# Kernel optimization log

Hardware: AMD Instinct MI355X
Metric: run time of the kernel (lower is better)

Reference implementation:

```python
import jax, jax.numpy as jnp
from jax import lax
import numpy as np

# Mask type 'A' for 7x7 conv: rows above center, left of center in center row; center excluded.
_m = np.zeros((7, 7), np.float32)
_m[:3, :] = 1.0
_m[3, :3] = 1.0
MASK_A = jnp.asarray(_m)


def masked_conv7(x, w, b):
    # x: [B,1,H,W], w: [16,1,7,7]
    wm = w * MASK_A[None, None]
    y = lax.conv_general_dilated(x, wm, (1, 1), [(3, 3), (3, 3)],
                                 dimension_numbers=("NCHW", "OIHW", "NCHW"))
    return y + b[None, :, None, None]


def skew(x):
    # [B,C,H,W] -> [B,C,H,H+W-1], row i shifted right by i (diagonals -> columns)
    B, C, H, W = x.shape
    rows = jnp.arange(H)[:, None]
    cols = rows + jnp.arange(W)[None, :]
    out = jnp.zeros((B, C, H, H + W - 1), x.dtype)
    return out.at[:, :, rows, cols].set(x)


def unskew(xs, W):
    B, C, H, _ = xs.shape
    rows = jnp.arange(H)[:, None]
    cols = rows + jnp.arange(W)[None, :]
    return xs[:, :, rows, cols]


def diag_lstm(x, wi, bi, ws0, ws1):
    # One direction of the diagonal LSTM. x: [B,16,H,W]
    B, C, H, W = x.shape
    xs = skew(x)  # [B,16,H,T], T = H+W-1
    # 1x1 input-to-state conv over the whole skewed map (precomputed)
    i2s = jnp.einsum("oc,bcht->boht", wi, xs) + bi[None, :, None, None]  # [B,64,H,T]

    def step(carry, col):
        h, c = carry  # [B,16,H] each
        # 2x1 state-to-state conv along height (causal downward): taps h[i], h[i-1]
        h_up = jnp.pad(h, ((0, 0), (0, 0), (1, 0)))[:, :, :-1]
        s = col + jnp.einsum("oc,bch->boh", ws1, h) + jnp.einsum("oc,bch->boh", ws0, h_up)
        o, f, i, g = jnp.split(s, 4, axis=1)
        c = jax.nn.sigmoid(f) * c + jax.nn.sigmoid(i) * jnp.tanh(g)
        h = jax.nn.sigmoid(o) * jnp.tanh(c)
        return (h, c), h

    cols = jnp.moveaxis(i2s, 3, 0)  # [T,B,64,H]
    z = jnp.zeros((B, C, H), x.dtype)
    _, hs = lax.scan(step, (z, z), cols)  # [T,B,16,H]
    hs = jnp.moveaxis(hs, 0, 3)  # [B,16,H,T]
    return unskew(hs, W)


def bilstm_layer(x, wi2, bi2, w02, w12):
    fwd = diag_lstm(x, wi2[0], bi2[0], w02[0], w12[0])
    xr = x[:, :, :, ::-1]
    bwd = diag_lstm(xr, wi2[1], bi2[1], w02[1], w12[1])[:, :, :, ::-1]
    # shift right-to-left output down one row to preserve causality
    bwd = jnp.pad(bwd, ((0, 0), (0, 0), (1, 0), (0, 0)))[:, :, :-1, :]
    return x + fwd + bwd  # residual


def pixelrnn_fwd(X, conv_in_w, conv_in_b, rnn_i2s_w, rnn_i2s_b, rnn_ss_w0, rnn_ss_w1,
                 out_w1, out_b1, out_w2, out_b2, out_w3, out_b3):
    h = masked_conv7(X, conv_in_w, conv_in_b)
    for l in range(7):
        h = bilstm_layer(h, rnn_i2s_w[l], rnn_i2s_b[l], rnn_ss_w0[l], rnn_ss_w1[l])
    for w, b in ((out_w1, out_b1), (out_w2, out_b2)):
        h = jax.nn.relu(jnp.einsum("oc,bchw->bohw", w, h) + b[None, :, None, None])
    return jnp.einsum("oc,bchw->bohw", out_w3, h) + out_b3[None, :, None, None]


def setup_inputs() -> dict:
    key = jax.random.key(0)
    ks = jax.random.split(key, 10)
    B, H, W = 32, 64, 64
    s = 0.25  # ~1/sqrt(16) init scale
    return {
        "X": jax.random.normal(ks[0], (B, 1, H, W), jnp.float32),
        "conv_in_w": jax.random.normal(ks[1], (16, 1, 7, 7), jnp.float32) * 0.15,
        "conv_in_b": jnp.zeros((16,), jnp.float32),
        "rnn_i2s_w": jax.random.normal(ks[2], (7, 2, 64, 16), jnp.float32) * s,
        "rnn_i2s_b": jnp.zeros((7, 2, 64), jnp.float32),
        "rnn_ss_w0": jax.random.normal(ks[3], (7, 2, 64, 16), jnp.float32) * s,
        "rnn_ss_w1": jax.random.normal(ks[4], (7, 2, 64, 16), jnp.float32) * s,
        "out_w1": jax.random.normal(ks[5], (16, 16), jnp.float32) * s,
        "out_b1": jnp.zeros((16,), jnp.float32),
        "out_w2": jax.random.normal(ks[6], (16, 16), jnp.float32) * s,
        "out_b2": jnp.zeros((16,), jnp.float32),
        "out_w3": jax.random.normal(ks[7], (1, 16), jnp.float32) * s,
        "out_b3": jnp.zeros((1,), jnp.float32),
    }


def reference(X, conv_in_w, conv_in_b, rnn_i2s_w, rnn_i2s_b, rnn_ss_w0, rnn_ss_w1,
              out_w1, out_b1, out_w2, out_b2, out_w3, out_b3):
    return pixelrnn_fwd(X, conv_in_w, conv_in_b, rnn_i2s_w, rnn_i2s_b, rnn_ss_w0,
                        rnn_ss_w1, out_w1, out_b1, out_w2, out_b2, out_w3, out_b3)
```

## Files before the change

kernel.cpp:

```cpp
#include <hip/hip_runtime.h>

#define DI __device__ __forceinline__

typedef __bf16 bf16x8 __attribute__((ext_vector_type(8)));
typedef float f32x4 __attribute__((ext_vector_type(4)));
typedef unsigned short u16x8 __attribute__((ext_vector_type(8)));
typedef unsigned short u16x4 __attribute__((ext_vector_type(4)));

DI float frcp(float x) { return __builtin_amdgcn_rcpf(x); }
DI float fsig(float x) { return frcp(1.0f + __expf(-x)); }
DI float ftanh(float x) { return 1.0f - 2.0f * frcp(1.0f + __expf(2.0f * x)); }

__global__ __launch_bounds__(256) void k_conv(const float* __restrict__ X,
                                              const float* __restrict__ Wc,
                                              const float* __restrict__ Bc,
                                              float* __restrict__ xo) {
    int n = blockIdx.x * 256 + threadIdx.x;
    int xx = n & 63, yy = (n >> 6) & 63, b = n >> 12;
    float acc[16];
#pragma unroll
    for (int o = 0; o < 16; ++o) acc[o] = Bc[o];
    const float* Xb = X + (size_t)b * 4096;
#pragma unroll
    for (int ky = 0; ky < 4; ++ky) {
        int yi = yy + ky - 3;
        if (yi < 0) continue;
        int kxmax = (ky == 3) ? 3 : 7;
        for (int kx = 0; kx < kxmax; ++kx) {
            int xi = xx + kx - 3;
            if (xi < 0 || xi > 63) continue;
            float v = Xb[yi * 64 + xi];
#pragma unroll
            for (int o = 0; o < 16; ++o)
                acc[o] = fmaf(Wc[o * 49 + ky * 7 + kx], v, acc[o]);
        }
    }
    float4* xp = reinterpret_cast<float4*>(xo + (size_t)n * 16);
#pragma unroll
    for (int q = 0; q < 4; ++q) {
        float4 t; t.x = acc[q*4]; t.y = acc[q*4+1]; t.z = acc[q*4+2]; t.w = acc[q*4+3];
        xp[q] = t;
    }
}

__global__ __launch_bounds__(256, 1) void k_scan(const float* __restrict__ Vin,
                                                 float* __restrict__ Vout,
                                                 const float* __restrict__ fwdIn,
                                                 const float* __restrict__ bwdIn,
                                                 float* __restrict__ fwdOut,
                                                 float* __restrict__ bwdOut,
                                                 const float* __restrict__ wi_all,
                                                 const float* __restrict__ w0_all,
                                                 const float* __restrict__ w1_all,
                                                 const float* __restrict__ bi_all,
                                                 int layer, int first) {
    int dir = blockIdx.x >> 5, b = blockIdx.x & 31;
    int t = threadIdx.x;
    int wv = t >> 6;
    int l = t & 63;
    int kb = l >> 4;
    int m = l & 15;
    int r = wv * 16 + m;
    int wb_ = (layer * 2 + dir) * 1024;

    const float* Wsel = (kb < 2 ? w1_all : w0_all) + wb_;
    int koff = (kb & 1) * 8;
    bf16x8 ahi[4], alo[4];
#pragma unroll
    for (int mb = 0; mb < 4; ++mb) {
        const float* wr = Wsel + (mb * 16 + m) * 16 + koff;
#pragma unroll
        for (int j = 0; j < 8; ++j) {
            float wv_ = wr[j];
            __bf16 hi = (__bf16)wv_;
            ahi[mb][j] = hi;
            alo[mb][j] = (__bf16)(wv_ - (float)hi);
        }
    }

    const float* Wi = wi_all + wb_;
    int cbase = (kb & 1) * 8;
    bf16x8 wihi[4], wiloz[4];
#pragma unroll
    for (int mb = 0; mb < 4; ++mb) {
        const float* wr = Wi + (mb * 16 + m) * 16 + cbase;
#pragma unroll
        for (int j = 0; j < 8; ++j) {
            float wv_ = wr[j];
            __bf16 hi = (__bf16)wv_;
            wihi[mb][j] = hi;
            wiloz[mb][j] = (kb < 2) ? (__bf16)(wv_ - (float)hi) : (__bf16)0.f;
        }
    }

    f32x4 biasv[4];
#pragma unroll
    for (int mb = 0; mb < 4; ++mb)
#pragma unroll
        for (int j = 0; j < 4; ++j)
            biasv[mb][j] = bi_all[(layer * 2 + dir) * 64 + mb * 16 + kb * 4 + j];

    __shared__ __align__(16) unsigned short hbuf[2][2][65 * 24];
    for (int i = t; i < 2 * 2 * 65 * 24; i += 256) (&hbuf[0][0][0])[i] = 0;

    const size_t rowbase  = ((size_t)b * 64 + r) * 64;
    const size_t rowbaseU = ((size_t)b * 64 + (r - 1)) * 64;
    float* ob = dir ? bwdOut : fwdOut;
    bool vstore_lane = (!first) && (dir == 0) && (kb < 2);
    bool fb_load = !first;
    bool b_load = fb_load && (r > 0);

    float cst[4] = {0.f, 0.f, 0.f, 0.f};

    f32x4 xc[2], fc[2], bc[2];
    {
        int w = 0 - r;
        bool valid = (unsigned)w < 64u;
#pragma unroll
        for (int q = 0; q < 2; ++q) { xc[q] = (f32x4){0,0,0,0}; fc[q] = (f32x4){0,0,0,0}; bc[q] = (f32x4){0,0,0,0}; }
        if (valid) {
            int wimg = dir ? (63 - w) : w;
            const f32x4* px = reinterpret_cast<const f32x4*>(Vin + (rowbase + wimg) * 16 + cbase);
            xc[0] = px[0]; xc[1] = px[1];
            if (fb_load) {
                const f32x4* pf = reinterpret_cast<const f32x4*>(fwdIn + (rowbase + wimg) * 16 + cbase);
                fc[0] = pf[0]; fc[1] = pf[1];
                if (b_load) {
                    const f32x4* pb = reinterpret_cast<const f32x4*>(bwdIn + (rowbaseU + wimg) * 16 + cbase);
                    bc[0] = pb[0]; bc[1] = pb[1];
                }
            }
        }
    }
    __syncthreads();

    int p = 0;
#pragma unroll 1
    for (int tt = 0; tt < 127; ++tt) {
        f32x4 xn[2], fn[2], bn[2];
#pragma unroll
        for (int q = 0; q < 2; ++q) { xn[q] = (f32x4){0,0,0,0}; fn[q] = (f32x4){0,0,0,0}; bn[q] = (f32x4){0,0,0,0}; }
        {
            int w = tt + 1 - r;
            if ((unsigned)w < 64u) {
                int wimg = dir ? (63 - w) : w;
                const f32x4* px = reinterpret_cast<const f32x4*>(Vin + (rowbase + wimg) * 16 + cbase);
                xn[0] = px[0]; xn[1] = px[1];
                if (fb_load) {
                    const f32x4* pf = reinterpret_cast<const f32x4*>(fwdIn + (rowbase + wimg) * 16 + cbase);
                    fn[0] = pf[0]; fn[1] = pf[1];
                    if (b_load) {
                        const f32x4* pb = reinterpret_cast<const f32x4*>(bwdIn + (rowbaseU + wimg) * 16 + cbase);
                        bn[0] = pb[0]; bn[1] = pb[1];
                    }
                }
            }
        }

        int wcur = tt - r;
        bool vout = (unsigned)wcur < 64u;
        int wo = dir ? (63 - wcur) : wcur;

        f32x4 v8[2];
#pragma unroll
        for (int q = 0; q < 2; ++q) v8[q] = xc[q] + fc[q] + bc[q];
        bf16x8 vsel;
#pragma unroll
        for (int q = 0; q < 2; ++q)
#pragma unroll
            for (int j = 0; j < 4; ++j) {
                float f = v8[q][j];
                __bf16 hi = (__bf16)f;
                vsel[q * 4 + j] = (kb < 2) ? hi : (__bf16)(f - (float)hi);
            }
        if (vstore_lane && vout) {
            f32x4* pv = reinterpret_cast<f32x4*>(Vout + (rowbase + wo) * 16 + cbase);
            pv[0] = v8[0]; pv[1] = v8[1];
        }

        f32x4 acc[4];
#pragma unroll
        for (int mb = 0; mb < 4; ++mb) acc[mb] = biasv[mb];
#pragma unroll
        for (int mb = 0; mb < 4; ++mb)
            acc[mb] = __builtin_amdgcn_mfma_f32_16x16x32_bf16(wihi[mb], vsel, acc[mb], 0, 0, 0);
#pragma unroll
        for (int mb = 0; mb < 4; ++mb)
            acc[mb] = __builtin_amdgcn_mfma_f32_16x16x32_bf16(wiloz[mb], vsel, acc[mb], 0, 0, 0);

        int q = r + 1 - (kb >> 1);
        int boff = q * 24 + (kb & 1) * 8;
        u16x8 bh_raw = *reinterpret_cast<const u16x8*>(&hbuf[p][0][boff]);
        u16x8 bl_raw = *reinterpret_cast<const u16x8*>(&hbuf[p][1][boff]);
        bf16x8 bhi = __builtin_bit_cast(bf16x8, bh_raw);
        bf16x8 blo = __builtin_bit_cast(bf16x8, bl_raw);
#pragma unroll
        for (int mb = 0; mb < 4; ++mb)
            acc[mb] = __builtin_amdgcn_mfma_f32_16x16x32_bf16(ahi[mb], bhi, acc[mb], 0, 0, 0);
#pragma unroll
        for (int mb = 0; mb < 4; ++mb)
            acc[mb] = __builtin_amdgcn_mfma_f32_16x16x32_bf16(ahi[mb], blo, acc[mb], 0, 0, 0);
#pragma unroll
        for (int mb = 0; mb < 4; ++mb)
            acc[mb] = __builtin_amdgcn_mfma_f32_16x16x32_bf16(alo[mb], bhi, acc[mb], 0, 0, 0);

        float hv[4];
        u16x4 hih, lol;
#pragma unroll
        for (int j = 0; j < 4; ++j) {
            float so = acc[0][j], sf = acc[1][j], si = acc[2][j], sg = acc[3][j];
            float cn = fsig(sf) * cst[j] + fsig(si) * ftanh(sg);
            cst[j] = cn;
            float hn = fsig(so) * ftanh(cn);
            hv[j] = hn;
            __bf16 hi = (__bf16)hn;
            hih[j] = __builtin_bit_cast(unsigned short, hi);
            lol[j] = __builtin_bit_cast(unsigned short, (__bf16)(hn - (float)hi));
        }
        int widx = (r + 1) * 24 + kb * 4;
        *reinterpret_cast<u16x4*>(&hbuf[p ^ 1][0][widx]) = hih;
        *reinterpret_cast<u16x4*>(&hbuf[p ^ 1][1][widx]) = lol;
        if (vout) {
            float4 hq; hq.x = hv[0]; hq.y = hv[1]; hq.z = hv[2]; hq.w = hv[3];
            *reinterpret_cast<float4*>(ob + (rowbase + wo) * 16 + kb * 4) = hq;
        }
#pragma unroll
        for (int qq = 0; qq < 2; ++qq) { xc[qq] = xn[qq]; fc[qq] = fn[qq]; bc[qq] = bn[qq]; }

        asm volatile("s_waitcnt lgkmcnt(0)" ::: "memory");
        __builtin_amdgcn_sched_barrier(0);
        __builtin_amdgcn_s_barrier();
        __builtin_amdgcn_sched_barrier(0);
        p ^= 1;
    }
}

__global__ __launch_bounds__(256) void k_head(const float* __restrict__ x,
                                              const float* __restrict__ fwd,
                                              const float* __restrict__ bwdr,
                                              const float* __restrict__ W1,
                                              const float* __restrict__ B1,
                                              const float* __restrict__ W2,
                                              const float* __restrict__ B2,
                                              const float* __restrict__ W3,
                                              const float* __restrict__ B3,
                                              float* __restrict__ out) {
    int n = blockIdx.x * 256 + threadIdx.x;
    int r = (n >> 6) & 63;
    size_t pix = (size_t)n;
    float v[16];
    const float4* xp = reinterpret_cast<const float4*>(x + pix * 16);
#pragma unroll
    for (int q = 0; q < 4; ++q) {
        float4 t = xp[q];
        v[q*4] = t.x; v[q*4+1] = t.y; v[q*4+2] = t.z; v[q*4+3] = t.w;
    }
    const float4* fp = reinterpret_cast<const float4*>(fwd + pix * 16);
#pragma unroll
    for (int q = 0; q < 4; ++q) {
        float4 t = fp[q];
        v[q*4] += t.x; v[q*4+1] += t.y; v[q*4+2] += t.z; v[q*4+3] += t.w;
    }
    if (r > 0) {
        const float4* bp = reinterpret_cast<const float4*>(bwdr + (pix - 64) * 16);
#pragma unroll
        for (int q = 0; q < 4; ++q) {
            float4 t = bp[q];
            v[q*4] += t.x; v[q*4+1] += t.y; v[q*4+2] += t.z; v[q*4+3] += t.w;
        }
    }
    float h1[16];
#pragma unroll
    for (int o = 0; o < 16; ++o) {
        float a = B1[o];
#pragma unroll
        for (int c = 0; c < 16; ++c) a = fmaf(W1[o * 16 + c], v[c], a);
        h1[o] = fmaxf(a, 0.f);
    }
    float h2[16];
#pragma unroll
    for (int o = 0; o < 16; ++o) {
        float a = B2[o];
#pragma unroll
        for (int c = 0; c < 16; ++c) a = fmaf(W2[o * 16 + c], h1[c], a);
        h2[o] = fmaxf(a, 0.f);
    }
    float y = B3[0];
#pragma unroll
    for (int c = 0; c < 16; ++c) y = fmaf(W3[c], h2[c], y);
    out[pix] = y;
}

extern "C" void kernel_launch(void* const* d_in, const int* in_sizes, int n_in,
                              void* d_out, int out_size, void* d_ws, size_t ws_size,
                              hipStream_t stream) {
    const float* X  = (const float*)d_in[0];
    const float* cw = (const float*)d_in[1];
    const float* cb = (const float*)d_in[2];
    const float* wi = (const float*)d_in[3];
    const float* bi = (const float*)d_in[4];
    const float* w0 = (const float*)d_in[5];
    const float* w1 = (const float*)d_in[6];
    const float* W1 = (const float*)d_in[7];
    const float* B1 = (const float*)d_in[8];
    const float* W2 = (const float*)d_in[9];
    const float* B2 = (const float*)d_in[10];
    const float* W3 = (const float*)d_in[11];
    const float* B3 = (const float*)d_in[12];
    float* out = (float*)d_out;

    char* ws = (char*)d_ws;
    float* V0 = (float*)ws;
    float* V1 = (float*)(ws + ((size_t)8 << 20));
    float* f0 = (float*)(ws + ((size_t)16 << 20));
    float* b0 = (float*)(ws + ((size_t)24 << 20));
    float* f1 = (float*)(ws + ((size_t)32 << 20));
    float* b1 = (float*)(ws + ((size_t)40 << 20));

    k_conv<<<512, 256, 0, stream>>>(X, cw, cb, V0);
    for (int l = 0; l < 7; ++l) {
        const float* Vin = (l == 0) ? V0 : (((l - 1) & 1) ? V1 : V0);
        float* Vout = (l == 0) ? V1 : ((l & 1) ? V1 : V0);
        const float* fIn = ((l + 1) & 1) ? f1 : f0;
        const float* bIn = ((l + 1) & 1) ? b1 : b0;
        float* fOut = (l & 1) ? f1 : f0;
        float* bOut = (l & 1) ? b1 : b0;
        k_scan<<<64, 256, 0, stream>>>(Vin, Vout, fIn, bIn, fOut, bOut,
                                       wi, w0, w1, bi, l, l == 0 ? 1 : 0);
    }
    k_head<<<512, 256, 0, stream>>>(V0, f0, b0, W1, B1, W2, B2, W3, B3, out);
}
```

Baseline: 1.004 ms.

## Replace per-step block barrier with point-to-point wave flags in LSTM scan

The per-timestep __syncthreads in the diagonal LSTM scan is replaced by producer/consumer flag spinning between adjacent waves. A 4-deep LDS ring buffer for h lets waves run up to a few steps apart. Branchy guarded global loads and stores become unconditional pointer-stepped accesses that are redirected to a zero buffer or a dump buffer when out of range, and the loop is unrolled by four. The aim is to cut barrier stalls and branch overhead on the serial critical path. The cost is spin-wait polling on volatile LDS flags, which carries ordering and correctness risks, plus extra wasted memory traffic to the dummy buffers.

```diff
diff --git a/kernel.cpp b/kernel.cpp
--- a/kernel.cpp
+++ b/kernel.cpp
@@ -10,6 +10,10 @@
 DI float frcp(float x) { return __builtin_amdgcn_rcpf(x); }
 DI float fsig(float x) { return frcp(1.0f + __expf(-x)); }
 DI float ftanh(float x) { return 1.0f - 2.0f * frcp(1.0f + __expf(2.0f * x)); }
+
+__global__ __launch_bounds__(256) void k_zero(float* __restrict__ zp) {
+    zp[threadIdx.x] = 0.f;
+}
 
 __global__ __launch_bounds__(256) void k_conv(const float* __restrict__ X,
                                               const float* __restrict__ Wc,
@@ -45,15 +49,17 @@
 
 __global__ __launch_bounds__(256, 1) void k_scan(const float* __restrict__ Vin,
                                                  float* __restrict__ Vout,
-                                                 const float* __restrict__ fwdIn,
-                                                 const float* __restrict__ bwdIn,
-                                                 float* __restrict__ fwdOut,
-                                                 float* __restrict__ bwdOut,
+                                                 const float* __restrict__ fIn,
+                                                 const float* __restrict__ bIn,
+                                                 float* __restrict__ fOut,
+                                                 float* __restrict__ bOut,
                                                  const float* __restrict__ wi_all,
                                                  const float* __restrict__ w0_all,
                                                  const float* __restrict__ w1_all,
                                                  const float* __restrict__ bi_all,
-                                                 int layer, int first) {
+                                                 int layer, int first,
+                                                 const float* __restrict__ zp,
+                                                 float* __restrict__ dump) {
     int dir = blockIdx.x >> 5, b = blockIdx.x & 31;
     int t = threadIdx.x;
     int wv = t >> 6;
@@ -77,7 +83,6 @@
             alo[mb][j] = (__bf16)(wv_ - (float)hi);
         }
     }
-
     const float* Wi = wi_all + wb_;
     int cbase = (kb & 1) * 8;
     bf16x8 wihi[4], wiloz[4];
@@ -92,7 +97,6 @@
             wiloz[mb][j] = (kb < 2) ? (__bf16)(wv_ - (float)hi) : (__bf16)0.f;
         }
     }
-
     f32x4 biasv[4];
 #pragma unroll
     for (int mb = 0; mb < 4; ++mb)
@@ -100,139 +104,155 @@
         for (int j = 0; j < 4; ++j)
             biasv[mb][j] = bi_all[(layer * 2 + dir) * 64 + mb * 16 + kb * 4 + j];
 
-    __shared__ __align__(16) unsigned short hbuf[2][2][65 * 24];
-    for (int i = t; i < 2 * 2 * 65 * 24; i += 256) (&hbuf[0][0][0])[i] = 0;
-
-    const size_t rowbase  = ((size_t)b * 64 + r) * 64;
-    const size_t rowbaseU = ((size_t)b * 64 + (r - 1)) * 64;
-    float* ob = dir ? bwdOut : fwdOut;
-    bool vstore_lane = (!first) && (dir == 0) && (kb < 2);
+    __shared__ __align__(16) unsigned short hbuf[4][2][65 * 24];
+    __shared__ unsigned pf[4];
+    __shared__ unsigned cf[4];
+    for (int i = t; i < 4 * 2 * 65 * 24; i += 256) (&hbuf[0][0][0])[i] = 0;
+    if (t < 4) { pf[t] = 0; cf[t] = 0; }
+
+    volatile unsigned* pfw = pf + (wv > 0 ? wv - 1 : 0);
+    volatile unsigned* cfn = cf + (wv < 3 ? wv + 1 : 3);
+    volatile unsigned* cfp = cf + wv;
+    volatile unsigned* pfp = pf + wv;
+
+    const size_t rowbase = ((size_t)b * 64 + r) * 64;
+    const size_t rowbaseU = (r > 0) ? rowbase - 64 : rowbase;
+    const int wimg0 = dir ? (63 + r) : (0 - r);
+    const long st4 = dir ? -4 : 4;
     bool fb_load = !first;
     bool b_load = fb_load && (r > 0);
+    bool vlane = fb_load && (dir == 0) && (kb < 2);
+
+    const f32x4* zp4 = (const f32x4*)zp;
+    const f32x4* pX = (const f32x4*)(Vin + ((long)rowbase + wimg0) * 16 + cbase);
+    const f32x4* pF = fb_load ? (const f32x4*)(fIn + ((long)rowbase + wimg0) * 16 + cbase) : zp4;
+    const f32x4* pB = b_load ? (const f32x4*)(bIn + ((long)rowbaseU + wimg0) * 16 + cbase) : zp4;
+    const long stF = fb_load ? st4 : 0;
+    const long stB = b_load ? st4 : 0;
+
+    float* ob = dir ? bOut : fOut;
+    f32x4* dumpT = (f32x4*)(dump + (size_t)t * 16);
+    f32x4* pH = (f32x4*)(ob + ((long)rowbase + wimg0) * 16 + kb * 4);
+    f32x4* pV = vlane ? (f32x4*)(Vout + ((long)rowbase + wimg0) * 16 + cbase) : dumpT;
+    const long stV = vlane ? st4 : 0;
+
+    const int boff = (r + 1 - (kb >> 1)) * 24 + (kb & 1) * 8;
+    const int widx = (r + 1) * 24 + kb * 4;
 
     float cst[4] = {0.f, 0.f, 0.f, 0.f};
 
-    f32x4 xc[2], fc[2], bc[2];
+    f32x4 xc0, xc1, fc0, fc1, bc0, bc1;
     {
-        int w = 0 - r;
-        bool valid = (unsigned)w < 64u;
-#pragma unroll
-        for (int q = 0; q < 2; ++q) { xc[q] = (f32x4){0,0,0,0}; fc[q] = (f32x4){0,0,0,0}; bc[q] = (f32x4){0,0,0,0}; }
-        if (valid) {
-            int wimg = dir ? (63 - w) : w;
-            const f32x4* px = reinterpret_cast<const f32x4*>(Vin + (rowbase + wimg) * 16 + cbase);
-            xc[0] = px[0]; xc[1] = px[1];
-            if (fb_load) {
-                const f32x4* pf = reinterpret_cast<const f32x4*>(fwdIn + (rowbase + wimg) * 16 + cbase);
-                fc[0] = pf[0]; fc[1] = pf[1];
-                if (b_load) {
-                    const f32x4* pb = reinterpret_cast<const f32x4*>(bwdIn + (rowbaseU + wimg) * 16 + cbase);
-                    bc[0] = pb[0]; bc[1] = pb[1];
-                }
-            }
-        }
-    }
+        bool lv0 = (r == 0);
+        const f32x4* ax = lv0 ? pX : zp4;
+        const f32x4* af = lv0 ? pF : zp4;
+        const f32x4* ab = lv0 ? pB : zp4;
+        xc0 = ax[0]; xc1 = ax[1];
+        fc0 = af[0]; fc1 = af[1];
+        bc0 = ab[0]; bc1 = ab[1];
+    }
+    int wnt = 1 - r;
     __syncthreads();
 
-    int p = 0;
+#define SCAN_BODY(TT, SR, SW)                                                     \
+    {                                                                             \
+                                         \
+        pX += st4; pF += stF; pB += stB;                                          \
+        bool lv = (unsigned)wnt < 64u;                                            \
+        const f32x4* ax = lv ? pX : zp4;                                          \
+        const f32x4* af = lv ? pF : zp4;                                          \
+        const f32x4* ab = lv ? pB : zp4;                                          \
+        f32x4 xn0 = ax[0], xn1 = ax[1];                                           \
+        f32x4 fn0 = af[0], fn1 = af[1];                                           \
+        f32x4 bn0 = ab[0], bn1 = ab[1];                                           \
+        bool sv = (unsigned)(wnt - 1) < 64u;                                      \
+                                              \
+        f32x4 v80 = xc0 + fc0 + bc0, v81 = xc1 + fc1 + bc1;                       \
+        bf16x8 vsel;                                                              \
+        _Pragma("unroll")                                                         \
+        for (int j = 0; j < 4; ++j) {                                             \
+            float f0v = v80[j], f1v = v81[j];                                     \
+            __bf16 h0 = (__bf16)f0v, h1 = (__bf16)f1v;                            \
+            vsel[j]     = (kb < 2) ? h0 : (__bf16)(f0v - (float)h0);              \
+            vsel[4 + j] = (kb < 2) ? h1 : (__bf16)(f1v - (float)h1);              \
+        }                                                                         \
+        {                                                                         \
+            f32x4* vd = sv ? pV : dumpT;                                          \
+            vd[0] = v80; vd[1] = v81;                                             \
+        }                                                                         \
+                                                        \
+        f32x4 acc[4];                                                             \
+        _Pragma("unroll")                                                         \
+        for (int mb = 0; mb < 4; ++mb) acc[mb] = biasv[mb];                       \
+        _Pragma("unroll")                                                         \
+        for (int mb = 0; mb < 4; ++mb)                                            \
+            acc[mb] = __builtin_amdgcn_mfma_f32_16x16x32_bf16(wihi[mb], vsel, acc[mb], 0, 0, 0); \
+        _Pragma("unroll")                                                         \
+        for (int mb = 0; mb < 4; ++mb)                                            \
+            acc[mb] = __builtin_amdgcn_mfma_f32_16x16x32_bf16(wiloz[mb], vsel, acc[mb], 0, 0, 0); \
+                            \
+        if (wv > 0) {                                                             \
+            while (*pfw < (unsigned)(TT)) __builtin_amdgcn_s_sleep(2);            \
+            __builtin_amdgcn_sched_barrier(0);                                    \
+        }                                                                         \
+        u16x8 bh_raw = *(const u16x8*)&hbuf[SR][0][boff];                         \
+        u16x8 bl_raw = *(const u16x8*)&hbuf[SR][1][boff];                         \
+        __builtin_amdgcn_sched_barrier(0);                                        \
+        if (wv > 0 && l == 0) *cfp = (unsigned)(TT) + 1u;                         \
+        bf16x8 bhi = __builtin_bit_cast(bf16x8, bh_raw);                          \
+        bf16x8 blo = __builtin_bit_cast(bf16x8, bl_raw);                          \
+        _Pragma("unroll")                                                         \
+        for (int mb = 0; mb < 4; ++mb)                                            \
+            acc[mb] = __builtin_amdgcn_mfma_f32_16x16x32_bf16(ahi[mb], bhi, acc[mb], 0, 0, 0); \
+        _Pragma("unroll")                                                         \
+        for (int mb = 0; mb < 4; ++mb)                                            \
+            acc[mb] = __builtin_amdgcn_mfma_f32_16x16x32_bf16(ahi[mb], blo, acc[mb], 0, 0, 0); \
+        _Pragma("unroll")                                                         \
+        for (int mb = 0; mb < 4; ++mb)                                            \
+            acc[mb] = __builtin_amdgcn_mfma_f32_16x16x32_bf16(alo[mb], bhi, acc[mb], 0, 0, 0); \
+                                                                    \
+        f32x4 hq;                                                                 \
+        u16x4 hih, lol;                                                           \
+        _Pragma("unroll")                                                         \
+        for (int j = 0; j < 4; ++j) {                                             \
+            float so = acc[0][j], sf = acc[1][j], si = acc[2][j], sg = acc[3][j]; \
+            float cn = fsig(sf) * cst[j] + fsig(si) * ftanh(sg);                  \
+            cst[j] = cn;                                                          \
+            float hn = fsig(so) * ftanh(cn);                                      \
+            hq[j] = hn;                                                           \
+            __bf16 hi = (__bf16)hn;                                               \
+            hih[j] = __builtin_bit_cast(unsigned short, hi);                      \
+            lol[j] = __builtin_bit_cast(unsigned short, (__bf16)(hn - (float)hi)); \
+        }                                                                         \
+                  \
+        if (wv < 3) {                                                             \
+            while ((int)*cfn < (TT) - 2) __builtin_amdgcn_s_sleep(2);             \
+            __builtin_amdgcn_sched_barrier(0);                                    \
+        }                                                                         \
+        *(u16x4*)&hbuf[SW][0][widx] = hih;                                        \
+        *(u16x4*)&hbuf[SW][1][widx] = lol;                                        \
+        __builtin_amdgcn_sched_barrier(0);                                        \
+        if (wv < 3 && l == 0) *pfp = (unsigned)(TT) + 1u;                         \
+                                                                  \
+        {                                                                         \
+            f32x4* hd = sv ? pH : dumpT;                                          \
+            hd[0] = hq;                                                           \
+        }                                                                         \
+                                                                   \
+        xc0 = xn0; xc1 = xn1; fc0 = fn0; fc1 = fn1; bc0 = bn0; bc1 = bn1;         \
+        pH += st4; pV += stV;                                                     \
+        ++wnt;                                                                    \
+    }
+
 #pragma unroll 1
-    for (int tt = 0; tt < 127; ++tt) {
-        f32x4 xn[2], fn[2], bn[2];
-#pragma unroll
-        for (int q = 0; q < 2; ++q) { xn[q] = (f32x4){0,0,0,0}; fn[q] = (f32x4){0,0,0,0}; bn[q] = (f32x4){0,0,0,0}; }
-        {
-            int w = tt + 1 - r;
-            if ((unsigned)w < 64u) {
-                int wimg = dir ? (63 - w) : w;
-                const f32x4* px = reinterpret_cast<const f32x4*>(Vin + (rowbase + wimg) * 16 + cbase);
-                xn[0] = px[0]; xn[1] = px[1];
-                if (fb_load) {
-                    const f32x4* pf = reinterpret_cast<const f32x4*>(fwdIn + (rowbase + wimg) * 16 + cbase);
-                    fn[0] = pf[0]; fn[1] = pf[1];
-                    if (b_load) {
-                        const f32x4* pb = reinterpret_cast<const f32x4*>(bwdIn + (rowbaseU + wimg) * 16 + cbase);
-                        bn[0] = pb[0]; bn[1] = pb[1];
-                    }
-                }
-            }
-        }
-
-        int wcur = tt - r;
-        bool vout = (unsigned)wcur < 64u;
-        int wo = dir ? (63 - wcur) : wcur;
-
-        f32x4 v8[2];
-#pragma unroll
-        for (int q = 0; q < 2; ++q) v8[q] = xc[q] + fc[q] + bc[q];
-        bf16x8 vsel;
-#pragma unroll
-        for (int q = 0; q < 2; ++q)
-#pragma unroll
-            for (int j = 0; j < 4; ++j) {
-                float f = v8[q][j];
-                __bf16 hi = (__bf16)f;
-                vsel[q * 4 + j] = (kb < 2) ? hi : (__bf16)(f - (float)hi);
-            }
-        if (vstore_lane && vout) {
-            f32x4* pv = reinterpret_cast<f32x4*>(Vout + (rowbase + wo) * 16 + cbase);
-            pv[0] = v8[0]; pv[1] = v8[1];
-        }
-
-        f32x4 acc[4];
-#pragma unroll
-        for (int mb = 0; mb < 4; ++mb) acc[mb] = biasv[mb];
-#pragma unroll
-        for (int mb = 0; mb < 4; ++mb)
-            acc[mb] = __builtin_amdgcn_mfma_f32_16x16x32_bf16(wihi[mb], vsel, acc[mb], 0, 0, 0);
-#pragma unroll
-        for (int mb = 0; mb < 4; ++mb)
-            acc[mb] = __builtin_amdgcn_mfma_f32_16x16x32_bf16(wiloz[mb], vsel, acc[mb], 0, 0, 0);
-
-        int q = r + 1 - (kb >> 1);
-        int boff = q * 24 + (kb & 1) * 8;
-        u16x8 bh_raw = *reinterpret_cast<const u16x8*>(&hbuf[p][0][boff]);
-        u16x8 bl_raw = *reinterpret_cast<const u16x8*>(&hbuf[p][1][boff]);
-        bf16x8 bhi = __builtin_bit_cast(bf16x8, bh_raw);
-        bf16x8 blo = __builtin_bit_cast(bf16x8, bl_raw);
-#pragma unroll
-        for (int mb = 0; mb < 4; ++mb)
-            acc[mb] = __builtin_amdgcn_mfma_f32_16x16x32_bf16(ahi[mb], bhi, acc[mb], 0, 0, 0);
-#pragma unroll
-        for (int mb = 0; mb < 4; ++mb)
-            acc[mb] = __builtin_amdgcn_mfma_f32_16x16x32_bf16(ahi[mb], blo, acc[mb], 0, 0, 0);
-#pragma unroll
-        for (int mb = 0; mb < 4; ++mb)
-            acc[mb] = __builtin_amdgcn_mfma_f32_16x16x32_bf16(alo[mb], bhi, acc[mb], 0, 0, 0);
-
-        float hv[4];
-        u16x4 hih, lol;
-#pragma unroll
-        for (int j = 0; j < 4; ++j) {
-            float so = acc[0][j], sf = acc[1][j], si = acc[2][j], sg = acc[3][j];
-            float cn = fsig(sf) * cst[j] + fsig(si) * ftanh(sg);
-            cst[j] = cn;
-            float hn = fsig(so) * ftanh(cn);
-            hv[j] = hn;
-            __bf16 hi = (__bf16)hn;
-            hih[j] = __builtin_bit_cast(unsigned short, hi);
-            lol[j] = __builtin_bit_cast(unsigned short, (__bf16)(hn - (float)hi));
-        }
-        int widx = (r + 1) * 24 + kb * 4;
-        *reinterpret_cast<u16x4*>(&hbuf[p ^ 1][0][widx]) = hih;
-        *reinterpret_cast<u16x4*>(&hbuf[p ^ 1][1][widx]) = lol;
-        if (vout) {
-            float4 hq; hq.x = hv[0]; hq.y = hv[1]; hq.z = hv[2]; hq.w = hv[3];
-            *reinterpret_cast<float4*>(ob + (rowbase + wo) * 16 + kb * 4) = hq;
-        }
-#pragma unroll
-        for (int qq = 0; qq < 2; ++qq) { xc[qq] = xn[qq]; fc[qq] = fn[qq]; bc[qq] = bn[qq]; }
-
-        asm volatile("s_waitcnt lgkmcnt(0)" ::: "memory");
-        __builtin_amdgcn_sched_barrier(0);
-        __builtin_amdgcn_s_barrier();
-        __builtin_amdgcn_sched_barrier(0);
-        p ^= 1;
-    }
+    for (int it = 0; it < 32; ++it) {
+        int tb = it * 4;
+        SCAN_BODY(tb + 0, 0, 1)
+        SCAN_BODY(tb + 1, 1, 2)
+        SCAN_BODY(tb + 2, 2, 3)
+        SCAN_BODY(tb + 3, 3, 0)
+    }
+#undef SCAN_BODY
 }
 
 __global__ __launch_bounds__(256) void k_head(const float* __restrict__ x,
@@ -316,7 +336,10 @@
     float* b0 = (float*)(ws + ((size_t)24 << 20));
     float* f1 = (float*)(ws + ((size_t)32 << 20));
     float* b1 = (float*)(ws + ((size_t)40 << 20));
-
+    float* zp = (float*)(ws + ((size_t)48 << 20));
+    float* dump = (float*)(ws + ((size_t)48 << 20) + 65536);
+
+    k_zero<<<1, 256, 0, stream>>>(zp);
     k_conv<<<512, 256, 0, stream>>>(X, cw, cb, V0);
     for (int l = 0; l < 7; ++l) {
         const float* Vin = (l == 0) ? V0 : (((l - 1) & 1) ? V1 : V0);
@@ -326,7 +349,7 @@
         float* fOut = (l & 1) ? f1 : f0;
         float* bOut = (l & 1) ? b1 : b0;
         k_scan<<<64, 256, 0, stream>>>(Vin, Vout, fIn, bIn, fOut, bOut,
-                                       wi, w0, w1, bi, l, l == 0 ? 1 : 0);
+                                       wi, w0, w1, bi, l, l == 0 ? 1 : 0, zp, dump);
     }
     k_head<<<512, 256, 0, stream>>>(V0, f0, b0, W1, B1, W2, B2, W3, B3, out);
 }
```

Result: slower. 1.163 ms (+15.8%).
